# Kernel optimization log

Hardware: AMD Instinct MI355X
Metric: run time of the kernel (lower is better)

## Reference

```python
import jax, jax.numpy as jnp
import numpy as np

N = 50000
D = 64
E = 600000
NNZ = 800000


def setup_inputs() -> dict:
    key = jax.random.key(0)
    ks = jax.random.split(key, 12)
    s = 1.0 / np.sqrt(D)
    return {
        "emb": jax.random.normal(ks[0], (N, D), jnp.float32) * s,
        "W1": jax.random.normal(ks[1], (D, 2 * D), jnp.float32) * s,
        "b1": jnp.zeros((2 * D,), jnp.float32),
        "W2": jax.random.normal(ks[2], (2 * D, D), jnp.float32) * (1.0 / np.sqrt(2 * D)),
        "b2": jnp.zeros((D,), jnp.float32),
        "gamma": jnp.ones((D,), jnp.float32),
        "beta": jnp.zeros((D,), jnp.float32),
        "hgc1_bias": jnp.zeros((D,), jnp.float32),
        "fc1_W": jax.random.normal(ks[3], (D, D), jnp.float32) * s,
        "fus_l1_W": jax.random.normal(ks[4], (D, D), jnp.float32) * s,
        "fus_l1_b": jnp.zeros((D,), jnp.float32),
        "fus_l2_W": jax.random.normal(ks[5], (1, D), jnp.float32) * s,
        "fus_l2_b": jnp.zeros((1,), jnp.float32),
        "hg_val": jax.random.uniform(ks[6], (NNZ,), jnp.float32) * 0.05,
        "edge_index": jax.random.randint(ks[7], (2, E), 0, N, jnp.int32),
        "hg_row": jax.random.randint(ks[8], (NNZ,), 0, N, jnp.int32),
        "hg_col": jax.random.randint(ks[9], (NNZ,), 0, N, jnp.int32),
    }


def gcn_conv(x, W, b, src, dst):
    # PyG-style GCNConv: add self loops, sym-normalized aggregation of x@W
    loop = jnp.arange(N, dtype=src.dtype)
    s = jnp.concatenate([src, loop])
    t = jnp.concatenate([dst, loop])
    deg = jax.ops.segment_sum(jnp.ones_like(t, jnp.float32), t, num_segments=N)
    dinv = jax.lax.rsqrt(jnp.maximum(deg, 1.0))
    norm = dinv[s] * dinv[t]                       # [E+N]
    xw = x @ W                                     # [N, out]
    msg = norm[:, None] * xw[s]                    # gather (irregular)
    return jax.ops.segment_sum(msg, t, num_segments=N) + b


def reference(emb, W1, b1, W2, b2, gamma, beta, hgc1_bias, fc1_W,
              fus_l1_W, fus_l1_b, fus_l2_W, fus_l2_b, hg_val,
              edge_index, hg_row, hg_col):
    src, dst = edge_index[0], edge_index[1]
    # ---- GraphNN: two GCN layers + BatchNorm (batch stats, eval dropout) ----
    h1 = gcn_conv(emb, W1, b1, src, dst)           # [N, 2D]
    h2 = gcn_conv(h1, W2, b2, src, dst)            # [N, D]
    mu = jnp.mean(h2, axis=0)
    var = jnp.var(h2, axis=0)
    hidden = (h2 - mu) * jax.lax.rsqrt(var + 1e-5) * gamma + beta
    # ---- HGNN2 / HGNN_conv: edge = G.T@x ; x = G@edge (sparse matmuls) ----
    x = jax.nn.relu(hidden) + hgc1_bias
    edge_emb = jax.ops.segment_sum(hg_val[:, None] * x[hg_row], hg_col, num_segments=N)
    x = jax.ops.segment_sum(hg_val[:, None] * edge_emb[hg_col], hg_row, num_segments=N)
    x = jax.nn.softmax(x, axis=1)
    sub_node = x @ fc1_W.T                         # fc1 (no bias)
    # ---- Fusion gate over {hidden, sub_node} ----
    stacked = jnp.stack([hidden, sub_node], axis=0)          # [2, N, D]
    g = jnp.tanh(stacked @ fus_l1_W.T + fus_l1_b)
    score = jax.nn.softmax(g @ fus_l2_W.T + fus_l2_b, axis=0)  # [2, N, 1]
    out = jnp.sum(score * stacked, axis=0)                   # [N, D]
    return out
```

## Files before the change

### kernel.cpp

```cpp
#include <hip/hip_runtime.h>
#include <hip/hip_fp16.h>


#define SEGSH 8
#define MAXSEG 256
#define PBLK 256

__device__ __forceinline__ float fast_tanh(float x) {
    float xc = fminf(fmaxf(x, -15.f), 15.f);
    float e = __expf(2.f * xc);
    return (e - 1.f) / (e + 1.f);
}

__global__ __launch_bounds__(256) void p1_count_kernel(const int* __restrict__ dst, int e,
                                                       const int* __restrict__ row,
                                                       const int* __restrict__ col, int nnz,
                                                       int* __restrict__ blockcnt, int nseg) {
    __shared__ int lc[3 * MAXSEG];
    for (int i = threadIdx.x; i < 3 * nseg; i += 256) lc[i] = 0;
    __syncthreads();
    int ce = (e + PBLK - 1) / PBLK;
    int cz = (nnz + PBLK - 1) / PBLK;
    int e0 = blockIdx.x * ce, e1 = min(e0 + ce, e);
    for (int i = e0 + threadIdx.x; i < e1; i += 256)
        atomicAdd(&lc[dst[i] >> SEGSH], 1);
    int z0 = blockIdx.x * cz, z1 = min(z0 + cz, nnz);
    for (int i = z0 + threadIdx.x; i < z1; i += 256) {
        atomicAdd(&lc[nseg + (col[i] >> SEGSH)], 1);
        atomicAdd(&lc[2 * nseg + (row[i] >> SEGSH)], 1);
    }
    __syncthreads();
    for (int r = threadIdx.x; r < 3 * nseg; r += 256)
        blockcnt[r * PBLK + blockIdx.x] = lc[r];
}

__global__ __launch_bounds__(256) void p2a_kernel(int* __restrict__ blockcnt,
                                                  int* __restrict__ segtot, int rows) {
    int rw = blockIdx.x * 4 + (threadIdx.x >> 6);
    if (rw >= rows) return;
    int ln = threadIdx.x & 63;
    int b = rw * PBLK + ln * 4;
    int v0 = blockcnt[b], v1 = blockcnt[b + 1], v2 = blockcnt[b + 2], v3 = blockcnt[b + 3];
    int s = v0 + v1 + v2 + v3;
    int incl = s;
    for (int d = 1; d < 64; d <<= 1) {
        int t = __shfl_up(incl, d, 64);
        if (ln >= d) incl += t;
    }
    int excl = incl - s;
    blockcnt[b]     = excl;
    blockcnt[b + 1] = excl + v0;
    blockcnt[b + 2] = excl + v0 + v1;
    blockcnt[b + 3] = excl + v0 + v1 + v2;
    if (ln == 63) segtot[rw] = incl;
}

__global__ __launch_bounds__(192) void p2b_kernel(const int* __restrict__ segtot,
                                                  int* __restrict__ segoff, int nseg) {
    int st = threadIdx.x >> 6, ln = threadIdx.x & 63;
    int chunk = (nseg + 63) / 64;
    int s0 = ln * chunk, s1 = min(s0 + chunk, nseg);
    int sum = 0;
    for (int i = s0; i < s1; ++i) sum += segtot[st * nseg + i];
    int incl = sum;
    for (int d = 1; d < 64; d <<= 1) {
        int v = __shfl_up(incl, d, 64);
        if (ln >= d) incl += v;
    }
    int run = incl - sum;
    for (int i = s0; i < s1; ++i) {
        segoff[st * nseg + i] = run;
        run += segtot[st * nseg + i];
    }
}

__global__ __launch_bounds__(256) void p3_scatter_kernel(const int* __restrict__ src,
                                                         const int* __restrict__ dst, int e,
                                                         const int* __restrict__ row,
                                                         const int* __restrict__ col,
                                                         const float* __restrict__ val, int nnz,
                                                         const int* __restrict__ blockcnt,
                                                         const int* __restrict__ segoff,
                                                         unsigned* __restrict__ runG,
                                                         uint2* __restrict__ runC,
                                                         uint2* __restrict__ runR, int nseg) {
    __shared__ int base[3 * MAXSEG];
    __shared__ int cnt[3 * MAXSEG];
    for (int i = threadIdx.x; i < 3 * nseg; i += 256) {
        base[i] = segoff[i] + blockcnt[i * PBLK + blockIdx.x];
        cnt[i] = 0;
    }
    __syncthreads();
    int ce = (e + PBLK - 1) / PBLK;
    int cz = (nnz + PBLK - 1) / PBLK;
    int e0 = blockIdx.x * ce, e1 = min(e0 + ce, e);
    for (int i = e0 + threadIdx.x; i < e1; i += 256) {
        int d = dst[i];
        int sg = d >> SEGSH;
        int p = atomicAdd(&cnt[sg], 1);
        runG[base[sg] + p] = ((unsigned)d << 16) | (unsigned)src[i];
    }
    int z0 = blockIdx.x * cz, z1 = min(z0 + cz, nnz);
    for (int i = z0 + threadIdx.x; i < z1; i += 256) {
        int r = row[i], c = col[i];
        unsigned hv = (unsigned)__half_as_ushort(__float2half(val[i]));
        int sgc = nseg + (c >> SEGSH);
        int p = atomicAdd(&cnt[sgc], 1);
        runC[base[sgc] + p] = make_uint2((unsigned)c, ((unsigned)r << 16) | hv);
        int sgr = 2 * nseg + (r >> SEGSH);
        p = atomicAdd(&cnt[sgr], 1);
        runR[base[sgr] + p] = make_uint2((unsigned)r, ((unsigned)c << 16) | hv);
    }
}

__global__ __launch_bounds__(256) void csr_build_kernel(const unsigned* __restrict__ runG,
                                                        const uint2* __restrict__ runC,
                                                        const uint2* __restrict__ runR,
                                                        const int* __restrict__ segoff,
                                                        const int* __restrict__ segtot,
                                                        int nseg, int n,
                                                        int* __restrict__ gcn_off,
                                                        int* __restrict__ hgc_off,
                                                        int* __restrict__ hgr_off,
                                                        float* __restrict__ dinv,
                                                        unsigned short* __restrict__ gsrcs,
                                                        unsigned* __restrict__ entc,
                                                        unsigned* __restrict__ entr) {
    __shared__ int cG[256], cC[256], cR[256];
    int s = blockIdx.x;
    int t = threadIdx.x;
    cG[t] = 0; cC[t] = 0; cR[t] = 0;
    __syncthreads();
    int oG = segoff[s],            nG = segtot[s];
    int oC = segoff[nseg + s],     nC = segtot[nseg + s];
    int oR = segoff[2 * nseg + s], nR = segtot[2 * nseg + s];
    for (int i = t; i < nG; i += 256) atomicAdd(&cG[(runG[oG + i] >> 16) & 255], 1);
    for (int i = t; i < nC; i += 256) atomicAdd(&cC[runC[oC + i].x & 255], 1);
    for (int i = t; i < nR; i += 256) atomicAdd(&cR[runR[oR + i].x & 255], 1);
    __syncthreads();
    int vG = cG[t], vC = cC[t], vR = cR[t];
    for (int d = 1; d < 256; d <<= 1) {
        int tG = (t >= d) ? cG[t - d] : 0;
        int tC = (t >= d) ? cC[t - d] : 0;
        int tR = (t >= d) ? cR[t - d] : 0;
        __syncthreads();
        cG[t] += tG; cC[t] += tC; cR[t] += tR;
        __syncthreads();
    }
    int eG = cG[t] - vG, eC = cC[t] - vC, eR = cR[t] - vR;
    int key = (s << SEGSH) + t;
    if (key < n) {
        gcn_off[key] = oG + eG;
        hgc_off[key] = oC + eC;
        hgr_off[key] = oR + eR;
        dinv[key] = rsqrtf((float)(vG + 1));
    }
    if (key == n) {
        gcn_off[n] = oG + eG;
        hgc_off[n] = oC + eC;
        hgr_off[n] = oR + eR;
    }
    if (s == nseg - 1 && t == 255 && ((n & 255) == 0)) {
        gcn_off[n] = oG + cG[255];
        hgc_off[n] = oC + cC[255];
        hgr_off[n] = oR + cR[255];
    }
    __syncthreads();
    cG[t] = oG + eG; cC[t] = oC + eC; cR[t] = oR + eR;
    __syncthreads();
    for (int i = t; i < nG; i += 256) {
        unsigned u = runG[oG + i];
        int p = atomicAdd(&cG[(u >> 16) & 255], 1);
        gsrcs[p] = (unsigned short)(u & 0xffffu);
    }
    for (int i = t; i < nC; i += 256) {
        uint2 u = runC[oC + i];
        int p = atomicAdd(&cC[u.x & 255], 1);
        entc[p] = u.y;
    }
    for (int i = t; i < nR; i += 256) {
        uint2 u = runR[oR + i];
        int p = atomicAdd(&cR[u.x & 255], 1);
        entr[p] = u.y;
    }
}

__global__ __launch_bounds__(64) void wprep_kernel(const float* __restrict__ W1,
                                                   const float* __restrict__ W2,
                                                   const float* __restrict__ b1,
                                                   float* __restrict__ W12,
                                                   float* __restrict__ bw) {
    int r = blockIdx.x;
    int c = threadIdx.x;
    const float* a = (r < 64) ? (W1 + r * 128) : b1;
    float acc = 0.f;
#pragma unroll 8
    for (int k = 0; k < 128; ++k) acc = fmaf(a[k], W2[k * 64 + c], acc);
    if (r < 64) W12[r * 64 + c] = acc;
    else bw[c] = acc;
}

template <bool SDI>
__global__ __launch_bounds__(256) void gcn_gather_kernel(const float* __restrict__ x,
                                                         const float* __restrict__ dinv,
                                                         const int* __restrict__ off,
                                                         const unsigned short* __restrict__ srcs,
                                                         float* __restrict__ out,
                                                         float* __restrict__ sdi, int n) {
    int node = blockIdx.x * 4 + (threadIdx.x >> 6);
    if (node >= n) return;
    int lane = threadIdx.x & 63;
    int sub = lane >> 4;
    int q = lane & 15;
    int e0 = off[node], e1 = off[node + 1];
    float4 acc = make_float4(0.f, 0.f, 0.f, 0.f);
    float dsum = 0.f;
    int e = e0 + sub;
    int s = (e < e1) ? (int)srcs[e] : 0;
    float ds = (e < e1) ? dinv[s] : 0.f;
    for (; e < e1; e += 4) {
        int sn = (e + 4 < e1) ? (int)srcs[e + 4] : 0;
        float dsn = (e + 4 < e1) ? dinv[sn] : 0.f;
        const float4 v = *(const float4*)(x + (long long)s * 64 + q * 4);
        acc.x = fmaf(ds, v.x, acc.x);
        acc.y = fmaf(ds, v.y, acc.y);
        acc.z = fmaf(ds, v.z, acc.z);
        acc.w = fmaf(ds, v.w, acc.w);
        dsum += ds;
        s = sn; ds = dsn;
    }
    acc.x += __shfl_xor(acc.x, 16, 64); acc.x += __shfl_xor(acc.x, 32, 64);
    acc.y += __shfl_xor(acc.y, 16, 64); acc.y += __shfl_xor(acc.y, 32, 64);
    acc.z += __shfl_xor(acc.z, 16, 64); acc.z += __shfl_xor(acc.z, 32, 64);
    acc.w += __shfl_xor(acc.w, 16, 64); acc.w += __shfl_xor(acc.w, 32, 64);
    if (SDI) { dsum += __shfl_xor(dsum, 16, 64); dsum += __shfl_xor(dsum, 32, 64); }
    if (sub == 0) {
        float dt = dinv[node];
        const float4 xs = *(const float4*)(x + (long long)node * 64 + q * 4);
        float4 o;
        o.x = dt * fmaf(dt, xs.x, acc.x);
        o.y = dt * fmaf(dt, xs.y, acc.y);
        o.z = dt * fmaf(dt, xs.z, acc.z);
        o.w = dt * fmaf(dt, xs.w, acc.w);
        *(float4*)(out + (long long)node * 64 + q * 4) = o;
        if (SDI && q == 0) sdi[node] = dt * (dt + dsum);
    }
}

#define GP 68
__global__ __launch_bounds__(256) void gemm_h2_kernel(const float* __restrict__ X,
                                                      const float* __restrict__ W12,
                                                      const float* __restrict__ bw,
                                                      const float* __restrict__ b2,
                                                      const float* __restrict__ sdi,
                                                      float* __restrict__ h2,
                                                      float* __restrict__ stats, int n) {
    __shared__ float Xs[64 * GP];
    __shared__ float WL[64 * GP];
    __shared__ float cadd[64], b2l[64];
    int t = threadIdx.x;
    int tx = t & 15, ty = t >> 4;
    int r0 = blockIdx.x * 64;
    if (t < 64) cadd[t] = bw[t];
    else if (t < 128) b2l[t - 64] = b2[t - 64];
    for (int f = t; f < 1024; f += 256) {
        int d = f >> 4, k4 = (f & 15) << 2;
        *(float4*)&WL[d * GP + k4] = *(const float4*)&W12[d * 64 + k4];
        int gr = r0 + d;
        float4 xv = make_float4(0.f, 0.f, 0.f, 0.f);
        if (gr < n) xv = *(const float4*)&X[(long long)gr * 64 + k4];
        *(float4*)&Xs[d * GP + k4] = xv;
    }
    __syncthreads();

    float4 acc[4];
#pragma unroll
    for (int ri = 0; ri < 4; ++ri) acc[ri] = make_float4(0.f, 0.f, 0.f, 0.f);
    for (int k = 0; k < 64; k += 4) {
        float4 w0 = *(float4*)&WL[(k + 0) * GP + 4 * tx];
        float4 w1 = *(float4*)&WL[(k + 1) * GP + 4 * tx];
        float4 w2v = *(float4*)&WL[(k + 2) * GP + 4 * tx];
        float4 w3 = *(float4*)&WL[(k + 3) * GP + 4 * tx];
#pragma unroll
        for (int ri = 0; ri < 4; ++ri) {
            float4 xv = *(float4*)&Xs[(4 * ty + ri) * GP + k];
            acc[ri].x = fmaf(xv.x, w0.x, fmaf(xv.y, w1.x, fmaf(xv.z, w2v.x, fmaf(xv.w, w3.x, acc[ri].x))));
            acc[ri].y = fmaf(xv.x, w0.y, fmaf(xv.y, w1.y, fmaf(xv.z, w2v.y, fmaf(xv.w, w3.y, acc[ri].y))));
            acc[ri].z = fmaf(xv.x, w0.z, fmaf(xv.y, w1.z, fmaf(xv.z, w2v.z, fmaf(xv.w, w3.z, acc[ri].z))));
            acc[ri].w = fmaf(xv.x, w0.w, fmaf(xv.y, w1.w, fmaf(xv.z, w2v.w, fmaf(xv.w, w3.w, acc[ri].w))));
        }
    }

    float ps[4] = {0.f, 0.f, 0.f, 0.f}, pq[4] = {0.f, 0.f, 0.f, 0.f};
    float ca[4] = {cadd[4 * tx], cadd[4 * tx + 1], cadd[4 * tx + 2], cadd[4 * tx + 3]};
    float bb[4] = {b2l[4 * tx], b2l[4 * tx + 1], b2l[4 * tx + 2], b2l[4 * tx + 3]};
#pragma unroll
    for (int ri = 0; ri < 4; ++ri) {
        int r = r0 + 4 * ty + ri;
        if (r < n) {
            float sd = sdi[r];
            float4 v;
            v.x = acc[ri].x + sd * ca[0] + bb[0];
            v.y = acc[ri].y + sd * ca[1] + bb[1];
            v.z = acc[ri].z + sd * ca[2] + bb[2];
            v.w = acc[ri].w + sd * ca[3] + bb[3];
            *(float4*)&h2[(long long)r * 64 + 4 * tx] = v;
            ps[0] += v.x; ps[1] += v.y; ps[2] += v.z; ps[3] += v.w;
            pq[0] += v.x * v.x; pq[1] += v.y * v.y; pq[2] += v.z * v.z; pq[3] += v.w * v.w;
        }
    }
    __syncthreads();
    float* lsum = Xs;
    float* lsq  = Xs + 1024;
#pragma unroll
    for (int di = 0; di < 4; ++di) {
        lsum[ty * 64 + 4 * tx + di] = ps[di];
        lsq[ty * 64 + 4 * tx + di]  = pq[di];
    }
    __syncthreads();
    if (t < 64) {
        float s = 0.f, s2 = 0.f;
#pragma unroll
        for (int g = 0; g < 16; ++g) {
            s += lsum[g * 64 + t];
            s2 += lsq[g * 64 + t];
        }
        atomicAdd(&stats[t], s);
        atomicAdd(&stats[64 + t], s2);
    }
}

template <bool BN>
__global__ __launch_bounds__(256) void hg_gather_kernel(const float* __restrict__ in,
                                                        const int* __restrict__ off,
                                                        const unsigned* __restrict__ ents,
                                                        const float* __restrict__ stats,
                                                        const float* __restrict__ gamma,
                                                        const float* __restrict__ beta,
                                                        const float* __restrict__ hbias,
                                                        float invN,
                                                        float* __restrict__ out, int n) {
    int node = blockIdx.x * 4 + (threadIdx.x >> 6);
    if (node >= n) return;
    int lane = threadIdx.x & 63;
    int sub = lane >> 4;
    int q = lane & 15;
    float sc[4], sh[4], hb[4];
    if (BN) {
#pragma unroll
        for (int c = 0; c < 4; ++c) {
            int col = q * 4 + c;
            float mu = stats[col] * invN;
            float var = stats[64 + col] * invN - mu * mu;
            float s = gamma[col] * rsqrtf(var + 1e-5f);
            sc[c] = s; sh[c] = beta[col] - mu * s; hb[c] = hbias[col];
        }
    }
    int e0 = off[node], e1 = off[node + 1];
    float4 acc = make_float4(0.f, 0.f, 0.f, 0.f);
    int e = e0 + sub;
    unsigned t = (e < e1) ? ents[e] : 0u;
    for (; e < e1; e += 4) {
        unsigned tn = (e + 4 < e1) ? ents[e + 4] : 0u;
        float vv = __half2float(__ushort_as_half((unsigned short)(t & 0xffffu)));
        float4 v = *(const float4*)(in + (long long)(t >> 16) * 64 + q * 4);
        if (BN) {
            v.x = fmaxf(fmaf(v.x, sc[0], sh[0]), 0.f) + hb[0];
            v.y = fmaxf(fmaf(v.y, sc[1], sh[1]), 0.f) + hb[1];
            v.z = fmaxf(fmaf(v.z, sc[2], sh[2]), 0.f) + hb[2];
            v.w = fmaxf(fmaf(v.w, sc[3], sh[3]), 0.f) + hb[3];
        }
        acc.x = fmaf(vv, v.x, acc.x);
        acc.y = fmaf(vv, v.y, acc.y);
        acc.z = fmaf(vv, v.z, acc.z);
        acc.w = fmaf(vv, v.w, acc.w);
        t = tn;
    }
    acc.x += __shfl_xor(acc.x, 16, 64); acc.x += __shfl_xor(acc.x, 32, 64);
    acc.y += __shfl_xor(acc.y, 16, 64); acc.y += __shfl_xor(acc.y, 32, 64);
    acc.z += __shfl_xor(acc.z, 16, 64); acc.z += __shfl_xor(acc.z, 32, 64);
    acc.w += __shfl_xor(acc.w, 16, 64); acc.w += __shfl_xor(acc.w, 32, 64);
    if (sub == 0) *(float4*)(out + (long long)node * 64 + q * 4) = acc;
}

#define TPAD 68
__device__ __forceinline__ float dot4(float4 a, float4 b) {
    return fmaf(a.x, b.x, fmaf(a.y, b.y, fmaf(a.z, b.z, a.w * b.w)));
}

__global__ __launch_bounds__(256) void tail_kernel(const float* __restrict__ x2,
                                                   const float* __restrict__ h2raw,
                                                   const float* __restrict__ fc1_W,
                                                   const float* __restrict__ fusW1,
                                                   const float* __restrict__ b1,
                                                   const float* __restrict__ w2,
                                                   const float* __restrict__ b2,
                                                   const float* __restrict__ stats,
                                                   const float* __restrict__ gamma,
                                                   const float* __restrict__ beta,
                                                   float invN,
                                                   float* __restrict__ out, int n) {
    __shared__ float A[64 * TPAD];
    __shared__ float Hs[64 * TPAD];
    __shared__ float WL[64 * TPAD];
    __shared__ float bsc[64], bsh[64];
    int t = threadIdx.x;
    int tx = t & 15, ty = t >> 4;
    int r0 = blockIdx.x * 64;

    if (t < 64) {
        float mu = stats[t] * invN;
        float var = stats[64 + t] * invN - mu * mu;
        float s = gamma[t] * rsqrtf(var + 1e-5f);
        bsc[t] = s; bsh[t] = beta[t] - mu * s;
    }
    __syncthreads();

    float b1d[4], w2d[4];
#pragma unroll
    for (int di = 0; di < 4; ++di) {
        b1d[di] = b1[tx + 16 * di];
        w2d[di] = w2[tx + 16 * di];
    }
    float b20 = b2[0];

    for (int f = t; f < 1024; f += 256) {
        int d = f >> 4, k4 = (f & 15) << 2;
        *(float4*)&WL[d * TPAD + k4] = *(const float4*)&fc1_W[d * 64 + k4];
        int gr = r0 + d;
        float4 hv = make_float4(0.f, 0.f, 0.f, 0.f);
        if (gr < n) {
            hv = *(const float4*)&h2raw[(long long)gr * 64 + k4];
            hv.x = fmaf(hv.x, bsc[k4],     bsh[k4]);
            hv.y = fmaf(hv.y, bsc[k4 + 1], bsh[k4 + 1]);
            hv.z = fmaf(hv.z, bsc[k4 + 2], bsh[k4 + 2]);
            hv.w = fmaf(hv.w, bsc[k4 + 3], bsh[k4 + 3]);
        }
        *(float4*)&Hs[d * TPAD + k4] = hv;
    }

#pragma unroll
    for (int ri = 0; ri < 4; ++ri) {
        int rl = 4 * ty + ri;
        int r = r0 + rl;
        bool ok = r < n;
        float vv[4];
#pragma unroll
        for (int di = 0; di < 4; ++di)
            vv[di] = ok ? x2[(long long)r * 64 + tx + 16 * di] : 0.f;
        float m = fmaxf(fmaxf(vv[0], vv[1]), fmaxf(vv[2], vv[3]));
        for (int s = 1; s < 16; s <<= 1) m = fmaxf(m, __shfl_xor(m, s, 16));
        float e0 = __expf(vv[0] - m), e1 = __expf(vv[1] - m);
        float e2 = __expf(vv[2] - m), e3 = __expf(vv[3] - m);
        float sm = e0 + e1 + e2 + e3;
        for (int s = 1; s < 16; s <<= 1) sm += __shfl_xor(sm, s, 16);
        float inv = 1.0f / sm;
        A[rl * TPAD + tx]      = e0 * inv;
        A[rl * TPAD + tx + 16] = e1 * inv;
        A[rl * TPAD + tx + 32] = e2 * inv;
        A[rl * TPAD + tx + 48] = e3 * inv;
    }
    __syncthreads();

    float sn[4][4];
#pragma unroll
    for (int ri = 0; ri < 4; ++ri)
#pragma unroll
        for (int di = 0; di < 4; ++di) sn[ri][di] = 0.f;
    for (int k = 0; k < 64; k += 4) {
        float4 p4[4], w4[4];
#pragma unroll
        for (int ri = 0; ri < 4; ++ri) p4[ri] = *(float4*)&A[(4 * ty + ri) * TPAD + k];
#pragma unroll
        for (int di = 0; di < 4; ++di) w4[di] = *(float4*)&WL[(tx + 16 * di) * TPAD + k];
#pragma unroll
        for (int ri = 0; ri < 4; ++ri)
#pragma unroll
            for (int di = 0; di < 4; ++di)
                sn[ri][di] += dot4(p4[ri], w4[di]);
    }
    __syncthreads();

#pragma unroll
    for (int ri = 0; ri < 4; ++ri)
#pragma unroll
        for (int di = 0; di < 4; ++di)
            A[(4 * ty + ri) * TPAD + tx + 16 * di] = sn[ri][di];
    for (int f = t; f < 1024; f += 256) {
        int d = f >> 4, k4 = (f & 15) << 2;
        *(float4*)&WL[d * TPAD + k4] = *(const float4*)&fusW1[d * 64 + k4];
    }
    __syncthreads();

    float aH[4][4], aS[4][4];
#pragma unroll
    for (int ri = 0; ri < 4; ++ri)
#pragma unroll
        for (int di = 0; di < 4; ++di) { aH[ri][di] = b1d[di]; aS[ri][di] = b1d[di]; }
    for (int k = 0; k < 64; k += 4) {
        float4 h4[4], s4[4], w4[4];
#pragma unroll
        for (int ri = 0; ri < 4; ++ri) {
            h4[ri] = *(float4*)&Hs[(4 * ty + ri) * TPAD + k];
            s4[ri] = *(float4*)&A[(4 * ty + ri) * TPAD + k];
        }
#pragma unroll
        for (int di = 0; di < 4; ++di) w4[di] = *(float4*)&WL[(tx + 16 * di) * TPAD + k];
#pragma unroll
        for (int ri = 0; ri < 4; ++ri)
#pragma unroll
            for (int di = 0; di < 4; ++di) {
                aH[ri][di] += dot4(h4[ri], w4[di]);
                aS[ri][di] += dot4(s4[ri], w4[di]);
            }
    }

#pragma unroll
    for (int ri = 0; ri < 4; ++ri) {
        int rl = 4 * ty + ri;
        int r = r0 + rl;
        float pH = 0.f, pS = 0.f;
#pragma unroll
        for (int di = 0; di < 4; ++di) {
            pH = fmaf(fast_tanh(aH[ri][di]), w2d[di], pH);
            pS = fmaf(fast_tanh(aS[ri][di]), w2d[di], pS);
        }
        for (int s = 1; s < 16; s <<= 1) {
            pH += __shfl_xor(pH, s, 16);
            pS += __shfl_xor(pS, s, 16);
        }
        pH += b20; pS += b20;
        float mx = fmaxf(pH, pS);
        float eH = __expf(pH - mx), eS = __expf(pS - mx);
        float inv = 1.0f / (eH + eS);
        if (r < n) {
#pragma unroll
            for (int di = 0; di < 4; ++di) {
                int d = tx + 16 * di;
                float hv = Hs[rl * TPAD + d];
                out[(long long)r * 64 + d] = (eH * hv + eS * sn[ri][di]) * inv;
            }
        }
    }
}

extern "C" void kernel_launch(void* const* d_in, const int* in_sizes, int n_in,
                              void* d_out, int out_size, void* d_ws, size_t ws_size,
                              hipStream_t stream) {
    const float* emb       = (const float*)d_in[0];
    const float* W1        = (const float*)d_in[1];
    const float* b1        = (const float*)d_in[2];
    const float* W2        = (const float*)d_in[3];
    const float* b2        = (const float*)d_in[4];
    const float* gamma     = (const float*)d_in[5];
    const float* beta      = (const float*)d_in[6];
    const float* hgc1_bias = (const float*)d_in[7];
    const float* fc1_W     = (const float*)d_in[8];
    const float* fus_l1_W  = (const float*)d_in[9];
    const float* fus_l1_b  = (const float*)d_in[10];
    const float* fus_l2_W  = (const float*)d_in[11];
    const float* fus_l2_b  = (const float*)d_in[12];
    const float* hg_val    = (const float*)d_in[13];
    const int*   edge_index= (const int*)d_in[14];
    const int*   hg_row    = (const int*)d_in[15];
    const int*   hg_col    = (const int*)d_in[16];

    const int N    = in_sizes[0] / 64;
    const int E    = in_sizes[14] / 2;
    const int NNZ  = in_sizes[13];
    const int Np   = (N + 3) & ~3;
    const int NSEG = (N + 255) >> 8;
    const int* src = edge_index;
    const int* dst = edge_index + E;

    float* ws      = (float*)d_ws;
    float* dinv    = ws;
    float* sdi     = dinv + Np;
    float* w12     = sdi + Np;
    float* bw      = w12 + 4096;
    float* stats   = bw + 64;
    int*   gcn_off = (int*)(stats + 128);
    int*   hgc_off = gcn_off + (Np + 4);
    int*   hgr_off = hgc_off + (Np + 4);
    int*   segtot  = hgr_off + (Np + 4);
    int*   segoff  = segtot + 3 * NSEG;
    int*   blockcnt= segoff + 3 * NSEG;
    unsigned short* gcn_srcs = (unsigned short*)(blockcnt + 3 * NSEG * PBLK);
    unsigned* hgc_ent = (unsigned*)(gcn_srcs + ((E + 1) & ~1));
    unsigned* hgr_ent = hgc_ent + NNZ;
    float* buf1    = (float*)(hgr_ent + NNZ);
    float* buf2    = buf1 + (size_t)128 * Np;

    const int Ep = (E + 1) & ~1;
    unsigned* runG = (unsigned*)buf1;
    uint2*    runC = (uint2*)(runG + Ep);
    uint2*    runR = runC + NNZ;

    float* tbuf = buf2;
    float* ubuf = buf1;
    float* h2   = buf1 + (size_t)64 * Np;
    float* eemb = buf2;
    float* x2   = buf1;
    float* out  = (float*)d_out;

    const float invN = 1.0f / (float)N;

    hipMemsetAsync(stats, 0, 128 * sizeof(float), stream);
    p1_count_kernel<<<PBLK, 256, 0, stream>>>(dst, E, hg_row, hg_col, NNZ, blockcnt, NSEG);
    p2a_kernel<<<(3 * NSEG + 3) / 4, 256, 0, stream>>>(blockcnt, segtot, 3 * NSEG);
    p2b_kernel<<<1, 192, 0, stream>>>(segtot, segoff, NSEG);
    p3_scatter_kernel<<<PBLK, 256, 0, stream>>>(src, dst, E, hg_row, hg_col, hg_val, NNZ,
                                                blockcnt, segoff, runG, runC, runR, NSEG);
    csr_build_kernel<<<NSEG, 256, 0, stream>>>(runG, runC, runR, segoff, segtot, NSEG, N,
                                               gcn_off, hgc_off, hgr_off, dinv,
                                               gcn_srcs, hgc_ent, hgr_ent);

    wprep_kernel<<<65, 64, 0, stream>>>(W1, W2, b1, w12, bw);
    gcn_gather_kernel<true><<<(N + 3) / 4, 256, 0, stream>>>(emb, dinv, gcn_off, gcn_srcs,
                                                             tbuf, sdi, N);
    gcn_gather_kernel<false><<<(N + 3) / 4, 256, 0, stream>>>(tbuf, dinv, gcn_off, gcn_srcs,
                                                              ubuf, nullptr, N);
    gemm_h2_kernel<<<(N + 63) / 64, 256, 0, stream>>>(ubuf, w12, bw, b2, sdi, h2, stats, N);

    hg_gather_kernel<true><<<(N + 3) / 4, 256, 0, stream>>>(h2, hgc_off, hgc_ent,
                                                            stats, gamma, beta, hgc1_bias,
                                                            invN, eemb, N);
    hg_gather_kernel<false><<<(N + 3) / 4, 256, 0, stream>>>(eemb, hgr_off, hgr_ent,
                                                             nullptr, nullptr, nullptr, nullptr,
                                                             0.f, x2, N);

    tail_kernel<<<(N + 63) / 64, 256, 0, stream>>>(x2, h2, fc1_W, fus_l1_W, fus_l1_b,
                                                   fus_l2_W, fus_l2_b, stats, gamma, beta,
                                                   invN, out, N);
}
```

Measured before the change: 290.1 us.

## Unroll gather loops by two edges and read tail weights from global cache

The GCN and hypergraph gather loops now handle two edges per iteration with independent loads, replacing the software-pipelined single-edge prefetch. This puts more memory requests in flight per thread. The tail kernel drops the shared-memory WL staging of fc1_W and fusW1 and reads the weights straight from global memory through the cache. That frees about 17 KB of LDS per block, which may allow more blocks per CU, at the cost of repeated global or L1 weight reads in the inner GEMM loops.

```diff
diff --git a/kernel.cpp b/kernel.cpp
--- a/kernel.cpp
+++ b/kernel.cpp
@@ -216,18 +216,27 @@
     float4 acc = make_float4(0.f, 0.f, 0.f, 0.f);
     float dsum = 0.f;
     int e = e0 + sub;
-    int s = (e < e1) ? (int)srcs[e] : 0;
-    float ds = (e < e1) ? dinv[s] : 0.f;
-    for (; e < e1; e += 4) {
-        int sn = (e + 4 < e1) ? (int)srcs[e + 4] : 0;
-        float dsn = (e + 4 < e1) ? dinv[sn] : 0.f;
-        const float4 v = *(const float4*)(x + (long long)s * 64 + q * 4);
-        acc.x = fmaf(ds, v.x, acc.x);
-        acc.y = fmaf(ds, v.y, acc.y);
-        acc.z = fmaf(ds, v.z, acc.z);
-        acc.w = fmaf(ds, v.w, acc.w);
-        dsum += ds;
-        s = sn; ds = dsn;
+    while (e + 4 < e1) {
+        int sa = srcs[e], sb = srcs[e + 4];
+        float da = dinv[sa], db = dinv[sb];
+        const float4 va = *(const float4*)(x + (long long)sa * 64 + q * 4);
+        const float4 vb = *(const float4*)(x + (long long)sb * 64 + q * 4);
+        acc.x = fmaf(da, va.x, fmaf(db, vb.x, acc.x));
+        acc.y = fmaf(da, va.y, fmaf(db, vb.y, acc.y));
+        acc.z = fmaf(da, va.z, fmaf(db, vb.z, acc.z));
+        acc.w = fmaf(da, va.w, fmaf(db, vb.w, acc.w));
+        dsum += da + db;
+        e += 8;
+    }
+    if (e < e1) {
+        int sa = srcs[e];
+        float da = dinv[sa];
+        const float4 va = *(const float4*)(x + (long long)sa * 64 + q * 4);
+        acc.x = fmaf(da, va.x, acc.x);
+        acc.y = fmaf(da, va.y, acc.y);
+        acc.z = fmaf(da, va.z, acc.z);
+        acc.w = fmaf(da, va.w, acc.w);
+        dsum += da;
     }
     acc.x += __shfl_xor(acc.x, 16, 64); acc.x += __shfl_xor(acc.x, 32, 64);
     acc.y += __shfl_xor(acc.y, 16, 64); acc.y += __shfl_xor(acc.y, 32, 64);
@@ -359,22 +368,42 @@
     int e0 = off[node], e1 = off[node + 1];
     float4 acc = make_float4(0.f, 0.f, 0.f, 0.f);
     int e = e0 + sub;
-    unsigned t = (e < e1) ? ents[e] : 0u;
-    for (; e < e1; e += 4) {
-        unsigned tn = (e + 4 < e1) ? ents[e + 4] : 0u;
-        float vv = __half2float(__ushort_as_half((unsigned short)(t & 0xffffu)));
-        float4 v = *(const float4*)(in + (long long)(t >> 16) * 64 + q * 4);
+    while (e + 4 < e1) {
+        unsigned ta = ents[e], tb = ents[e + 4];
+        float va_ = __half2float(__ushort_as_half((unsigned short)(ta & 0xffffu)));
+        float vb_ = __half2float(__ushort_as_half((unsigned short)(tb & 0xffffu)));
+        float4 a4 = *(const float4*)(in + (long long)(ta >> 16) * 64 + q * 4);
+        float4 b4 = *(const float4*)(in + (long long)(tb >> 16) * 64 + q * 4);
         if (BN) {
-            v.x = fmaxf(fmaf(v.x, sc[0], sh[0]), 0.f) + hb[0];
-            v.y = fmaxf(fmaf(v.y, sc[1], sh[1]), 0.f) + hb[1];
-            v.z = fmaxf(fmaf(v.z, sc[2], sh[2]), 0.f) + hb[2];
-            v.w = fmaxf(fmaf(v.w, sc[3], sh[3]), 0.f) + hb[3];
-        }
-        acc.x = fmaf(vv, v.x, acc.x);
-        acc.y = fmaf(vv, v.y, acc.y);
-        acc.z = fmaf(vv, v.z, acc.z);
-        acc.w = fmaf(vv, v.w, acc.w);
-        t = tn;
+            a4.x = fmaxf(fmaf(a4.x, sc[0], sh[0]), 0.f) + hb[0];
+            a4.y = fmaxf(fmaf(a4.y, sc[1], sh[1]), 0.f) + hb[1];
+            a4.z = fmaxf(fmaf(a4.z, sc[2], sh[2]), 0.f) + hb[2];
+            a4.w = fmaxf(fmaf(a4.w, sc[3], sh[3]), 0.f) + hb[3];
+            b4.x = fmaxf(fmaf(b4.x, sc[0], sh[0]), 0.f) + hb[0];
+            b4.y = fmaxf(fmaf(b4.y, sc[1], sh[1]), 0.f) + hb[1];
+            b4.z = fmaxf(fmaf(b4.z, sc[2], sh[2]), 0.f) + hb[2];
+            b4.w = fmaxf(fmaf(b4.w, sc[3], sh[3]), 0.f) + hb[3];
+        }
+        acc.x = fmaf(va_, a4.x, fmaf(vb_, b4.x, acc.x));
+        acc.y = fmaf(va_, a4.y, fmaf(vb_, b4.y, acc.y));
+        acc.z = fmaf(va_, a4.z, fmaf(vb_, b4.z, acc.z));
+        acc.w = fmaf(va_, a4.w, fmaf(vb_, b4.w, acc.w));
+        e += 8;
+    }
+    if (e < e1) {
+        unsigned ta = ents[e];
+        float va_ = __half2float(__ushort_as_half((unsigned short)(ta & 0xffffu)));
+        float4 a4 = *(const float4*)(in + (long long)(ta >> 16) * 64 + q * 4);
+        if (BN) {
+            a4.x = fmaxf(fmaf(a4.x, sc[0], sh[0]), 0.f) + hb[0];
+            a4.y = fmaxf(fmaf(a4.y, sc[1], sh[1]), 0.f) + hb[1];
+            a4.z = fmaxf(fmaf(a4.z, sc[2], sh[2]), 0.f) + hb[2];
+            a4.w = fmaxf(fmaf(a4.w, sc[3], sh[3]), 0.f) + hb[3];
+        }
+        acc.x = fmaf(va_, a4.x, acc.x);
+        acc.y = fmaf(va_, a4.y, acc.y);
+        acc.z = fmaf(va_, a4.z, acc.z);
+        acc.w = fmaf(va_, a4.w, acc.w);
     }
     acc.x += __shfl_xor(acc.x, 16, 64); acc.x += __shfl_xor(acc.x, 32, 64);
     acc.y += __shfl_xor(acc.y, 16, 64); acc.y += __shfl_xor(acc.y, 32, 64);
@@ -402,7 +431,6 @@
                                                    float* __restrict__ out, int n) {
     __shared__ float A[64 * TPAD];
     __shared__ float Hs[64 * TPAD];
-    __shared__ float WL[64 * TPAD];
     __shared__ float bsc[64], bsh[64];
     int t = threadIdx.x;
     int tx = t & 15, ty = t >> 4;
@@ -426,7 +454,6 @@
 
     for (int f = t; f < 1024; f += 256) {
         int d = f >> 4, k4 = (f & 15) << 2;
-        *(float4*)&WL[d * TPAD + k4] = *(const float4*)&fc1_W[d * 64 + k4];
         int gr = r0 + d;
         float4 hv = make_float4(0.f, 0.f, 0.f, 0.f);
         if (gr < n) {
@@ -472,7 +499,8 @@
 #pragma unroll
         for (int ri = 0; ri < 4; ++ri) p4[ri] = *(float4*)&A[(4 * ty + ri) * TPAD + k];
 #pragma unroll
-        for (int di = 0; di < 4; ++di) w4[di] = *(float4*)&WL[(tx + 16 * di) * TPAD + k];
+        for (int di = 0; di < 4; ++di)
+            w4[di] = *(const float4*)&fc1_W[(tx + 16 * di) * 64 + k];
 #pragma unroll
         for (int ri = 0; ri < 4; ++ri)
 #pragma unroll
@@ -486,10 +514,6 @@
 #pragma unroll
         for (int di = 0; di < 4; ++di)
             A[(4 * ty + ri) * TPAD + tx + 16 * di] = sn[ri][di];
-    for (int f = t; f < 1024; f += 256) {
-        int d = f >> 4, k4 = (f & 15) << 2;
-        *(float4*)&WL[d * TPAD + k4] = *(const float4*)&fusW1[d * 64 + k4];
-    }
     __syncthreads();
 
     float aH[4][4], aS[4][4];
@@ -505,7 +529,8 @@
             s4[ri] = *(float4*)&A[(4 * ty + ri) * TPAD + k];
         }
 #pragma unroll
-        for (int di = 0; di < 4; ++di) w4[di] = *(float4*)&WL[(tx + 16 * di) * TPAD + k];
+        for (int di = 0; di < 4; ++di)
+            w4[di] = *(const float4*)&fusW1[(tx + 16 * di) * 64 + k];
 #pragma unroll
         for (int ri = 0; ri < 4; ++ri)
 #pragma unroll
```

New measurement: 315.8 us. 1.09x slower.
